# Kernel optimization log

Hardware: AMD Instinct MI355X
Metric: run time of the kernel (lower is better)

## Reference

```python
import jax, jax.numpy as jnp
import numpy as np

H = 16  # num_heads


def setup_inputs() -> dict:
    key = jax.random.key(0)
    ks = jax.random.split(key, 8)
    B, S, d, L = 1, 2048, 1024, 8
    hd = d // H
    s = 0.02
    return {
        "x": jax.random.normal(ks[0], (B, S, d), jnp.float32),
        "past_values": jax.random.normal(ks[1], (L, B, H, S, hd), jnp.float32),
        "Wqkv": jax.random.normal(ks[2], (3 * d, d), jnp.float32) * s,
        "bqkv": jax.random.normal(ks[3], (3 * d,), jnp.float32) * s,
        "Wcol": jax.random.normal(ks[4], (d, d), jnp.float32) * s,
        "bcol": jax.random.normal(ks[5], (d,), jnp.float32) * s,
        "Wout": jax.random.normal(ks[6], (d, d), jnp.float32) * s,
        "bout": jax.random.normal(ks[7], (d,), jnp.float32) * s,
    }


def reference(x, past_values, Wqkv, bqkv, Wcol, bcol, Wout, bout):
    B, S, d = x.shape
    L = past_values.shape[0]
    hd = d // H
    scale = 1.0 / np.sqrt(hd).astype(np.float32)

    qkv = x @ Wqkv.T + bqkv                       # [B,S,3d]
    q, k, v = jnp.split(qkv, 3, axis=-1)

    def heads(t):                                  # [B,S,d] -> [B,H,S,hd]
        return t.reshape(B, S, H, hd).transpose(0, 2, 1, 3)

    q_row, k, v = heads(q), heads(k), heads(v)
    q_col = heads(x @ Wcol.T + bcol)

    # causal token scores [B,H,S,S]
    token_scores = jnp.einsum('bhqd,bhkd->bhqk', q_row, k) * scale
    causal = jnp.triu(jnp.ones((S, S), bool), 1)
    token_scores = jnp.where(causal, -jnp.inf, token_scores)

    # stack past values: torch stack(dim=3) -> [B,H,S,L,hd]; permute -> [B,S,L,H*hd]
    pv = past_values.transpose(1, 3, 0, 2, 4).reshape(B, S, L, d)
    ri = pv.reshape(B, S * L, d)
    mu = ri.mean(-1, keepdims=True)
    var = ri.var(-1, keepdims=True)
    ri = (ri - mu) / jnp.sqrt(var + 1e-5)          # F.layer_norm, no affine

    Wk, bk = Wqkv[d:2 * d], bqkv[d:2 * d]
    Wv, bv = Wqkv[2 * d:], bqkv[2 * d:]
    rk = (ri @ Wk.T + bk).reshape(B, S * L, H, hd).transpose(0, 2, 1, 3).reshape(B, H, S, L, hd)
    rv = (ri @ Wv.T + bv).reshape(B, S * L, H, hd).transpose(0, 2, 1, 3).reshape(B, H, S, L, hd)

    mem_scores = jnp.einsum('bhsd,bhsld->bhsl', q_col, rk) * scale  # [B,H,S,L]

    scores = jnp.concatenate([token_scores, mem_scores], axis=-1)   # [B,H,S,S+L]
    w = jax.nn.softmax(scores, axis=-1)
    tw, mw = w[..., :S], w[..., S:]

    ctx = jnp.einsum('bhqk,bhkd->bhqd', tw, v) + jnp.einsum('bhsl,bhsld->bhsd', mw, rv)
    out = ctx.transpose(0, 2, 1, 3).reshape(B, S, d)
    return out @ Wout.T + bout
```

## Files before the change

kernel.cpp:

```cpp
#include <hip/hip_runtime.h>
#include <math.h>

#define D   1024
#define H   16
#define HD  64
#define SEQ 2048
#define LL  8
#define SCALE 0.125f

typedef __attribute__((ext_vector_type(8))) __bf16 bf16x8;
typedef __attribute__((ext_vector_type(4))) float floatx4;
typedef __attribute__((ext_vector_type(8))) unsigned short ushort8;

__device__ inline unsigned short f32_to_bf16(float f) {
    unsigned int u = __builtin_bit_cast(unsigned int, f);
    u += 0x7FFF + ((u >> 16) & 1);
    return (unsigned short)(u >> 16);
}
__device__ inline float bf2f(unsigned short u) {
    unsigned int x = (unsigned int)u << 16;
    return __builtin_bit_cast(float, x);
}
__device__ inline void load_lds16(const void* g, void* l) {
    __builtin_amdgcn_global_load_lds(
        (__attribute__((address_space(1))) void*)g,
        (__attribute__((address_space(3))) void*)l, 16, 0, 0);
}

__device__ inline void xcd_swizzle(int& bx, int& by) {
    const int gx   = gridDim.x;
    const int lin  = blockIdx.y * gx + blockIdx.x;
    const int nblk = gx * gridDim.y;
    const int virt = (lin & 7) * (nblk >> 3) + (lin >> 3);
    bx = virt % gx;
    by = virt / gx;
}

#define NQ_X    524288
#define NQ_WQKV 786432
#define NQ_WC   262144
#define NQ_WO   262144
#define LN_BLK  16384
#define CVT_BLK 7168
#define PREP_GRID (LN_BLK + CVT_BLK + 4)

__global__ __launch_bounds__(256) void prep_kernel(
    const float* __restrict__ pv, const float* __restrict__ x,
    const float* __restrict__ Wqkv, const float* __restrict__ Wcol,
    const float* __restrict__ Wout, const float* __restrict__ bqkv,
    const float* __restrict__ bcol,
    unsigned short* __restrict__ ri, unsigned short* __restrict__ xb,
    unsigned short* __restrict__ W4b, unsigned short* __restrict__ Woutb,
    float* __restrict__ b4)
{
    const int b = blockIdx.x;
    const int t = threadIdx.x;
    if (b < LN_BLK) {
        const int r = b;
        const int s = r >> 3, l = r & 7;
        const int h = t >> 4, e = (t & 15) * 4;
        const size_t src = (size_t)l * (H * SEQ * HD) + (size_t)h * (SEQ * HD)
                         + (size_t)s * HD + e;
        float4 v = *(const float4*)(pv + src);
        float sum = v.x + v.y + v.z + v.w;
        float sq  = v.x * v.x + v.y * v.y + v.z * v.z + v.w * v.w;
#pragma unroll
        for (int off = 32; off; off >>= 1) {
            sum += __shfl_xor(sum, off);
            sq  += __shfl_xor(sq, off);
        }
        __shared__ float red[8];
        if ((t & 63) == 0) { red[(t >> 6) * 2] = sum; red[(t >> 6) * 2 + 1] = sq; }
        __syncthreads();
        sum = red[0] + red[2] + red[4] + red[6];
        sq  = red[1] + red[3] + red[5] + red[7];
        const float mean = sum * (1.f / 1024.f);
        const float var  = sq * (1.f / 1024.f) - mean * mean;
        const float rstd = rsqrtf(var + 1e-5f);
        ushort4 o;
        o.x = f32_to_bf16((v.x - mean) * rstd);
        o.y = f32_to_bf16((v.y - mean) * rstd);
        o.z = f32_to_bf16((v.z - mean) * rstd);
        o.w = f32_to_bf16((v.w - mean) * rstd);
        *(ushort4*)(ri + (size_t)r * D + t * 4) = o;
    } else if (b < LN_BLK + CVT_BLK) {
        const int i = (b - LN_BLK) * 256 + t;
        const float* src; unsigned short* dst; int off;
        if (i < NQ_X)                        { src = x;    dst = xb;    off = i; }
        else if (i < NQ_X + NQ_WQKV)         { src = Wqkv; dst = W4b;   off = i - NQ_X; }
        else if (i < NQ_X + NQ_WQKV + NQ_WC) { src = Wcol; dst = W4b;   off = i - NQ_X;
                                               src = Wcol; off = i - NQ_X - NQ_WQKV;
                                               dst = W4b + (size_t)NQ_WQKV * 4 / 1;
                                               {
                                                   float4 v = ((const float4*)Wcol)[i - NQ_X - NQ_WQKV];
                                                   ushort4 o;
                                                   o.x = f32_to_bf16(v.x); o.y = f32_to_bf16(v.y);
                                                   o.z = f32_to_bf16(v.z); o.w = f32_to_bf16(v.w);
                                                   ((ushort4*)(W4b))[NQ_WQKV + (i - NQ_X - NQ_WQKV)] = o;
                                               }
                                               return; }
        else                                 { src = Wout; dst = Woutb; off = i - NQ_X - NQ_WQKV - NQ_WC; }
        float4 v = ((const float4*)src)[off];
        ushort4 o;
        o.x = f32_to_bf16(v.x); o.y = f32_to_bf16(v.y);
        o.z = f32_to_bf16(v.z); o.w = f32_to_bf16(v.w);
        ((ushort4*)dst)[off] = o;
    } else {
        const int q = (b - LN_BLK - CVT_BLK) * 256 + t;
        float4 v = (q < 768) ? ((const float4*)bqkv)[q] : ((const float4*)bcol)[q - 768];
        ((float4*)b4)[q] = v;
    }
}

template <typename CT>
__global__ __launch_bounds__(256) void gemm_bf16_kernel(
    const unsigned short* __restrict__ A, const unsigned short* __restrict__ W,
    const float* __restrict__ bias, CT* __restrict__ C, int K, int N)
{
    __shared__ unsigned short As[128 * 32];
    __shared__ unsigned short Ws[128 * 32];
    const int t    = threadIdx.x;
    const int wave = t >> 6, lane = t & 63;
    const int wm   = wave >> 1, wn = wave & 1;
    int bx, by;
    xcd_swizzle(bx, by);
    const int m0 = by * 128, n0 = bx * 128;

    floatx4 acc[4][4];
#pragma unroll
    for (int i = 0; i < 4; i++)
#pragma unroll
        for (int j = 0; j < 4; j++) acc[i][j] = (floatx4)0.f;

    const int lrow = lane >> 2;
    const int lcol = (lane & 3) * 8;
    const unsigned short* Ag = A + (size_t)(m0 + wave * 32 + lrow) * K + lcol;
    const unsigned short* Wg = W + (size_t)(n0 + wave * 32 + lrow) * K + lcol;
    unsigned short* Asw = &As[wave * 32 * 32];
    unsigned short* Wsw = &Ws[wave * 32 * 32];
    const size_t rowskip = (size_t)16 * K;

    const int arow  = lane & 15;
    const int aquad = (lane >> 4) * 8;

    for (int k0 = 0; k0 < K; k0 += 32) {
        load_lds16(Ag + k0,           Asw);
        load_lds16(Ag + k0 + rowskip, Asw + 16 * 32);
        load_lds16(Wg + k0,           Wsw);
        load_lds16(Wg + k0 + rowskip, Wsw + 16 * 32);
        __syncthreads();

        bf16x8 af[4], wf[4];
#pragma unroll
        for (int mi = 0; mi < 4; mi++)
            af[mi] = *(const bf16x8*)&As[(wm * 64 + mi * 16 + arow) * 32 + aquad];
#pragma unroll
        for (int ni = 0; ni < 4; ni++)
            wf[ni] = *(const bf16x8*)&Ws[(wn * 64 + ni * 16 + arow) * 32 + aquad];
#pragma unroll
        for (int mi = 0; mi < 4; mi++)
#pragma unroll
            for (int ni = 0; ni < 4; ni++)
                acc[mi][ni] = __builtin_amdgcn_mfma_f32_16x16x32_bf16(
                    af[mi], wf[ni], acc[mi][ni], 0, 0, 0);
        __syncthreads();
    }

    const int crow = (lane >> 4) * 4, ccol = lane & 15;
#pragma unroll
    for (int mi = 0; mi < 4; mi++) {
#pragma unroll
        for (int ni = 0; ni < 4; ni++) {
            const int gm = m0 + wm * 64 + mi * 16 + crow;
            const int gn = n0 + wn * 64 + ni * 16 + ccol;
            const float bb = bias[gn];
#pragma unroll
            for (int r = 0; r < 4; r++) {
                float v = acc[mi][ni][r] + bb;
                if constexpr (sizeof(CT) == 2)
                    C[(size_t)(gm + r) * N + gn] = (CT)f32_to_bf16(v);
                else
                    C[(size_t)(gm + r) * N + gn] = v;
            }
        }
    }
}

union AttnShared {
    struct { unsigned short Qs[64 * 72]; unsigned short Ks[64 * 72]; } qk;
    float Osp[64 * 68];
};

__global__ __launch_bounds__(256) void attn_split_kernel(
    const unsigned short* __restrict__ qkv4, const unsigned short* __restrict__ rkv,
    float* __restrict__ Opart, float2* __restrict__ mlpart)
{
    const int t    = threadIdx.x;
    const int w    = t >> 6, lane = t & 63;
    const int lrow = lane & 15;
    const int lk   = (lane >> 4) * 8;
    const int rrow = (lane >> 4) * 4;
    const int lin  = blockIdx.x;
    const int hs   = lin & 31, g = lin >> 5;
    const int h    = hs >> 1, s = hs & 1;
    const int a    = g & 7, bq = g >> 3;
    const int qt   = (bq == 0) ? a : (bq == 1) ? 15 - a : (bq == 2) ? 16 + a : 31 - a;
    const int q0   = qt * 64;
    const int n    = qt + 1, nh = (n + 1) >> 1;
    const int lo   = s ? nh : 0, hi = s ? n : nh;
    const int part = (h * 32 + qt) * 2 + s;

    __shared__ AttnShared U;
    __shared__ unsigned short Vt[64 * 72];
    __shared__ unsigned short Pb[64 * 72];
    __shared__ float row_m[64], row_l[64];
    __shared__ float mem_mm[64], mem_alpha[64], mem_suml[64], mem_p[64 * 8];

#pragma unroll
    for (int p = 0; p < 2; p++) {
        int idx = p * 256 + t;
        int row = idx >> 3, col = (idx & 7) * 8;
        *(bf16x8*)&U.qk.Qs[row * 72 + col] =
            *(const bf16x8*)(qkv4 + (size_t)(q0 + row) * 4096 + h * HD + col);
    }

    float m_i[4], l_i[4];
    floatx4 Oacc[4];
#pragma unroll
    for (int r = 0; r < 4; r++) { m_i[r] = -1e30f; l_i[r] = 0.f; }
#pragma unroll
    for (int et = 0; et < 4; et++) Oacc[et] = (floatx4)0.f;

    for (int jt = lo; jt < hi; jt++) {
        const int j0 = jt * 64;
#pragma unroll
        for (int p = 0; p < 2; p++) {
            int idx = p * 256 + t;
            int row = idx >> 3, col = (idx & 7) * 8;
            *(bf16x8*)&U.qk.Ks[row * 72 + col] =
                *(const bf16x8*)(qkv4 + (size_t)(j0 + row) * 4096 + D + h * HD + col);
        }
        {
            const int pr = t & 31, eg = t >> 5;
            const unsigned short* v0 =
                qkv4 + (size_t)(j0 + 2 * pr) * 4096 + 2 * D + h * HD + eg * 8;
            ushort8 va = *(const ushort8*)v0;
            ushort8 vb = *(const ushort8*)(v0 + 4096);
#pragma unroll
            for (int j = 0; j < 8; j++) {
                unsigned int pk = (unsigned int)va[j] | ((unsigned int)vb[j] << 16);
                *(unsigned int*)&Vt[(eg * 8 + j) * 72 + 2 * pr] = pk;
            }
        }
        __syncthreads();

        floatx4 S[4];
#pragma unroll
        for (int nt = 0; nt < 4; nt++) S[nt] = (floatx4)0.f;
#pragma unroll
        for (int kst = 0; kst < 2; kst++) {
            bf16x8 aq = *(const bf16x8*)&U.qk.Qs[(w * 16 + lrow) * 72 + kst * 32 + lk];
#pragma unroll
            for (int nt = 0; nt < 4; nt++) {
                bf16x8 bk = *(const bf16x8*)&U.qk.Ks[(nt * 16 + lrow) * 72 + kst * 32 + lk];
                S[nt] = __builtin_amdgcn_mfma_f32_16x16x32_bf16(aq, bk, S[nt], 0, 0, 0);
            }
        }

#pragma unroll
        for (int r = 0; r < 4; r++) {
            const int qg = q0 + w * 16 + rrow + r;
            float sc[4];
            float mx = -1e30f;
#pragma unroll
            for (int nt = 0; nt < 4; nt++) {
                sc[nt] = S[nt][r] * SCALE;
                if (j0 + nt * 16 + lrow > qg) sc[nt] = -1e30f;
                mx = fmaxf(mx, sc[nt]);
            }
#pragma unroll
            for (int off = 1; off < 16; off <<= 1)
                mx = fmaxf(mx, __shfl_xor(mx, off));
            if (mx <= -1e29f) {
#pragma unroll
                for (int nt = 0; nt < 4; nt++)
                    Pb[(w * 16 + rrow + r) * 72 + nt * 16 + lrow] = 0;
                continue;
            }
            const float newm  = fmaxf(m_i[r], mx);
            const float alpha = __expf(m_i[r] - newm);
            m_i[r] = newm;
            float ps = 0.f;
#pragma unroll
            for (int nt = 0; nt < 4; nt++) {
                float pe = __expf(sc[nt] - newm);
                ps += pe;
                Pb[(w * 16 + rrow + r) * 72 + nt * 16 + lrow] = f32_to_bf16(pe);
            }
#pragma unroll
            for (int off = 1; off < 16; off <<= 1)
                ps += __shfl_xor(ps, off);
            l_i[r] = l_i[r] * alpha + ps;
#pragma unroll
            for (int et = 0; et < 4; et++) Oacc[et][r] *= alpha;
        }
        __syncthreads();

#pragma unroll
        for (int kst = 0; kst < 2; kst++) {
            bf16x8 ap = *(const bf16x8*)&Pb[(w * 16 + lrow) * 72 + kst * 32 + lk];
#pragma unroll
            for (int et = 0; et < 4; et++) {
                bf16x8 bv = *(const bf16x8*)&Vt[(et * 16 + lrow) * 72 + kst * 32 + lk];
                Oacc[et] = __builtin_amdgcn_mfma_f32_16x16x32_bf16(ap, bv, Oacc[et], 0, 0, 0);
            }
        }
        __syncthreads();
    }

    if (s == 1) {
#pragma unroll
        for (int r = 0; r < 4; r++) {
            const int ql = w * 16 + rrow + r;
            if (lrow == 0) mlpart[(size_t)part * 64 + ql] = make_float2(m_i[r], l_i[r]);
#pragma unroll
            for (int et = 0; et < 4; et++)
                Opart[((size_t)part * 64 + ql) * 64 + et * 16 + lrow] = Oacc[et][r];
        }
        return;
    }

#pragma unroll
    for (int r = 0; r < 4; r++) {
        const int ql = w * 16 + rrow + r;
        if (lrow == 0) { row_m[ql] = m_i[r]; row_l[ql] = l_i[r]; }
#pragma unroll
        for (int et = 0; et < 4; et++)
            U.Osp[ql * 68 + et * 16 + lrow] = Oacc[et][r];
    }
    __syncthreads();

    {
        const int qi = t >> 2, quad = t & 3;
        const int qg = q0 + qi;
        float qv[16];
        const unsigned short* qcp = qkv4 + (size_t)qg * 4096 + 3 * D + h * HD + quad * 16;
        ushort8 qa = *(const ushort8*)qcp;
        ushort8 qb = *(const ushort8*)(qcp + 8);
#pragma unroll
        for (int j = 0; j < 8; j++) {
            qv[j]     = bf2f(qa[j]) * SCALE;
            qv[8 + j] = bf2f(qb[j]) * SCALE;
        }
        float ms[8];
#pragma unroll
        for (int l = 0; l < 8; l++) {
            const unsigned short* rr = rkv + (size_t)(qg * LL + l) * 2048 + h * HD + quad * 16;
            ushort8 ra = *(const ushort8*)rr;
            ushort8 rb = *(const ushort8*)(rr + 8);
            float pacc = 0.f;
#pragma unroll
            for (int j = 0; j < 8; j++)
                pacc += qv[j] * bf2f(ra[j]) + qv[8 + j] * bf2f(rb[j]);
            pacc += __shfl_xor(pacc, 1);
            pacc += __shfl_xor(pacc, 2);
            ms[l] = pacc;
        }
        const float mo = row_m[qi];
        float mm = mo;
#pragma unroll
        for (int l = 0; l < 8; l++) mm = fmaxf(mm, ms[l]);
        const float alpha = __expf(mo - mm);
        float suml = 0.f;
        float pl[8];
#pragma unroll
        for (int l = 0; l < 8; l++) { pl[l] = __expf(ms[l] - mm); suml += pl[l]; }
        if (quad == 0) {
            mem_mm[qi]    = mm;
            mem_alpha[qi] = alpha;
            mem_suml[qi]  = suml;
#pragma unroll
            for (int l = 0; l < 8; l++) mem_p[qi * 8 + l] = pl[l];
        }
    }
    __syncthreads();

    {
        const int tx = t & 15, ty = t >> 4;
#pragma unroll
        for (int i = 0; i < 4; i++) {
            const int qi = ty * 4 + i, qg = q0 + qi;
            const float alpha = mem_alpha[qi];
            const float lf = row_l[qi] * alpha + mem_suml[qi];
            float4 o = *(const float4*)&U.Osp[qi * 68 + tx * 4];
            o.x *= alpha; o.y *= alpha; o.z *= alpha; o.w *= alpha;
#pragma unroll
            for (int l = 0; l < 8; l++) {
                const float p = mem_p[qi * 8 + l];
                ushort4 vb = *(const ushort4*)(rkv + (size_t)(qg * LL + l) * 2048
                                               + D + h * HD + tx * 4);
                o.x = fmaf(p, bf2f(vb.x), o.x);
                o.y = fmaf(p, bf2f(vb.y), o.y);
                o.z = fmaf(p, bf2f(vb.z), o.z);
                o.w = fmaf(p, bf2f(vb.w), o.w);
            }
            *(float4*)&Opart[((size_t)part * 64 + qi) * 64 + tx * 4] = o;
            if (tx == 0) mlpart[(size_t)part * 64 + qi] = make_float2(mem_mm[qi], lf);
        }
    }
}

__global__ __launch_bounds__(256) void attn_merge_kernel(
    const float* __restrict__ Opart, const float2* __restrict__ mlpart,
    unsigned short* __restrict__ ctx)
{
    const int blk = blockIdx.x;
    const int h = blk >> 5, qt = blk & 31;
    const int q0 = qt * 64;
    const int t = threadIdx.x, tx = t & 15, ty = t >> 4;
    const size_t p0 = (size_t)blk * 2, p1 = p0 + 1;
#pragma unroll
    for (int i = 0; i < 4; i++) {
        const int qi = ty * 4 + i, qg = q0 + qi;
        float2 ml0 = mlpart[p0 * 64 + qi];
        float2 ml1 = mlpart[p1 * 64 + qi];
        const float M  = fmaxf(ml0.x, ml1.x);
        const float f0 = __expf(ml0.x - M), f1 = __expf(ml1.x - M);
        const float rl = 1.f / (ml0.y * f0 + ml1.y * f1);
        float4 o0 = *(const float4*)&Opart[(p0 * 64 + qi) * 64 + tx * 4];
        float4 o1 = *(const float4*)&Opart[(p1 * 64 + qi) * 64 + tx * 4];
        ushort4 ob;
        ob.x = f32_to_bf16((o0.x * f0 + o1.x * f1) * rl);
        ob.y = f32_to_bf16((o0.y * f0 + o1.y * f1) * rl);
        ob.z = f32_to_bf16((o0.z * f0 + o1.z * f1) * rl);
        ob.w = f32_to_bf16((o0.w * f0 + o1.w * f1) * rl);
        *(ushort4*)(ctx + (size_t)qg * D + h * HD + tx * 4) = ob;
    }
}

extern "C" void kernel_launch(void* const* d_in, const int* in_sizes, int n_in,
                              void* d_out, int out_size, void* d_ws, size_t ws_size,
                              hipStream_t stream)
{
    const float* x    = (const float*)d_in[0];
    const float* pv   = (const float*)d_in[1];
    const float* Wqkv = (const float*)d_in[2];
    const float* bqkv = (const float*)d_in[3];
    const float* Wcol = (const float*)d_in[4];
    const float* bcol = (const float*)d_in[5];
    const float* Wout = (const float*)d_in[6];
    const float* bout = (const float*)d_in[7];
    float* out = (float*)d_out;

    char* p = (char*)d_ws;
    unsigned short* x_bf    = (unsigned short*)p; p += (size_t)2048 * 1024 * 2;
    unsigned short* W4_bf   = (unsigned short*)p; p += (size_t)4096 * 1024 * 2;
    unsigned short* Wout_bf = (unsigned short*)p; p += (size_t)1024 * 1024 * 2;
    float*          b4      = (float*)p;          p += (size_t)4096 * 4;
    unsigned short* ri_bf   = (unsigned short*)p; p += (size_t)16384 * 1024 * 2;
    unsigned short* qkv4_bf = (unsigned short*)p; p += (size_t)2048 * 4096 * 2;
    unsigned short* rkv_bf  = (unsigned short*)p; p += (size_t)16384 * 2048 * 2;
    unsigned short* ctx_bf  = (unsigned short*)p; p += (size_t)2048 * 1024 * 2;
    float*          Opart   = (float*)p;          p += (size_t)1024 * 64 * 64 * 4;
    float2*         mlpart  = (float2*)p;         p += (size_t)1024 * 64 * 8;

    prep_kernel<<<PREP_GRID, 256, 0, stream>>>(pv, x, Wqkv, Wcol, Wout, bqkv, bcol,
                                               ri_bf, x_bf, W4_bf, Wout_bf, b4);
    gemm_bf16_kernel<unsigned short><<<dim3(32, 16), 256, 0, stream>>>(
        x_bf, W4_bf, b4, qkv4_bf, 1024, 4096);
    gemm_bf16_kernel<unsigned short><<<dim3(16, 128), 256, 0, stream>>>(
        ri_bf, W4_bf + (size_t)1024 * 1024, bqkv + 1024, rkv_bf, 1024, 2048);
    attn_split_kernel<<<1024, 256, 0, stream>>>(qkv4_bf, rkv_bf, Opart, mlpart);
    attn_merge_kernel<<<512, 256, 0, stream>>>(Opart, mlpart, ctx_bf);
    gemm_bf16_kernel<float><<<dim3(8, 16), 256, 0, stream>>>(
        ctx_bf, Wout_bf, bout, out, 1024, 1024);
}
```

Baseline: 363.4 us.

## Fold memory K/V projections into attention via reassociation, drop rkv GEMM

Removes the large GEMM that projected all 16384 layer-normed past rows to K and V. A new mem_attn kernel instead folds Wk into the query (q·Wk_h, precomputed with a transposed Wk) and computes memory scores directly against the normalized rows. It then applies the softmax weights to those rows before multiplying by Wv, with bias terms handled analytically. The memory branch gets its own max/sum and is merged with the two token-attention partials in the merge kernel. This trades a 16384x2048x1024 GEMM and its large intermediate for smaller per-block MFMA work and an extra transpose in prep. The risk is large register arrays (z0/z1 of 64 floats each) and repeated reads of ri.

New measurement: 370.0 us. Within noise of the previous version (+1.8%).

```diff
diff --git a/kernel.cpp b/kernel.cpp
--- a/kernel.cpp
+++ b/kernel.cpp
@@ -7,6 +7,7 @@
 #define SEQ 2048
 #define LL  8
 #define SCALE 0.125f
+#define TZS 1048
 
 typedef __attribute__((ext_vector_type(8))) __bf16 bf16x8;
 typedef __attribute__((ext_vector_type(4))) float floatx4;
@@ -26,7 +27,6 @@
         (__attribute__((address_space(1))) void*)g,
         (__attribute__((address_space(3))) void*)l, 16, 0, 0);
 }
-
 __device__ inline void xcd_swizzle(int& bx, int& by) {
     const int gx   = gridDim.x;
     const int lin  = blockIdx.y * gx + blockIdx.x;
@@ -39,10 +39,10 @@
 #define NQ_X    524288
 #define NQ_WQKV 786432
 #define NQ_WC   262144
-#define NQ_WO   262144
 #define LN_BLK  16384
 #define CVT_BLK 7168
-#define PREP_GRID (LN_BLK + CVT_BLK + 4)
+#define TR_BLK  256
+#define PREP_GRID (LN_BLK + CVT_BLK + 4 + TR_BLK)
 
 __global__ __launch_bounds__(256) void prep_kernel(
     const float* __restrict__ pv, const float* __restrict__ x,
@@ -51,8 +51,9 @@
     const float* __restrict__ bcol,
     unsigned short* __restrict__ ri, unsigned short* __restrict__ xb,
     unsigned short* __restrict__ W4b, unsigned short* __restrict__ Woutb,
-    float* __restrict__ b4)
+    float* __restrict__ b4, unsigned short* __restrict__ WkT)
 {
+    __shared__ float ft[64][65];
     const int b = blockIdx.x;
     const int t = threadIdx.x;
     if (b < LN_BLK) {
@@ -86,29 +87,46 @@
     } else if (b < LN_BLK + CVT_BLK) {
         const int i = (b - LN_BLK) * 256 + t;
         const float* src; unsigned short* dst; int off;
-        if (i < NQ_X)                        { src = x;    dst = xb;    off = i; }
-        else if (i < NQ_X + NQ_WQKV)         { src = Wqkv; dst = W4b;   off = i - NQ_X; }
-        else if (i < NQ_X + NQ_WQKV + NQ_WC) { src = Wcol; dst = W4b;   off = i - NQ_X;
-                                               src = Wcol; off = i - NQ_X - NQ_WQKV;
-                                               dst = W4b + (size_t)NQ_WQKV * 4 / 1;
-                                               {
-                                                   float4 v = ((const float4*)Wcol)[i - NQ_X - NQ_WQKV];
-                                                   ushort4 o;
-                                                   o.x = f32_to_bf16(v.x); o.y = f32_to_bf16(v.y);
-                                                   o.z = f32_to_bf16(v.z); o.w = f32_to_bf16(v.w);
-                                                   ((ushort4*)(W4b))[NQ_WQKV + (i - NQ_X - NQ_WQKV)] = o;
-                                               }
-                                               return; }
-        else                                 { src = Wout; dst = Woutb; off = i - NQ_X - NQ_WQKV - NQ_WC; }
+        if (i < NQ_X) {
+            src = x; dst = xb; off = i;
+        } else if (i < NQ_X + NQ_WQKV) {
+            src = Wqkv; dst = W4b; off = i - NQ_X;
+        } else if (i < NQ_X + NQ_WQKV + NQ_WC) {
+            src = Wcol; dst = W4b + (size_t)NQ_WQKV * 4; off = i - NQ_X - NQ_WQKV;
+        } else {
+            src = Wout; dst = Woutb; off = i - NQ_X - NQ_WQKV - NQ_WC;
+        }
         float4 v = ((const float4*)src)[off];
         ushort4 o;
         o.x = f32_to_bf16(v.x); o.y = f32_to_bf16(v.y);
         o.z = f32_to_bf16(v.z); o.w = f32_to_bf16(v.w);
         ((ushort4*)dst)[off] = o;
-    } else {
+    } else if (b < LN_BLK + CVT_BLK + 4) {
         const int q = (b - LN_BLK - CVT_BLK) * 256 + t;
         float4 v = (q < 768) ? ((const float4*)bqkv)[q] : ((const float4*)bcol)[q - 768];
         ((float4*)b4)[q] = v;
+    } else {
+        const int tt = b - LN_BLK - CVT_BLK - 4;
+        const int kt = tt >> 4, et = tt & 15;
+        const int r = t >> 2, c16 = (t & 3) * 16;
+        const float* srow = Wqkv + (size_t)(1024 + et * 64 + r) * 1024 + kt * 64 + c16;
+#pragma unroll
+        for (int j = 0; j < 4; j++) {
+            float4 v = *(const float4*)(srow + j * 4);
+            ft[r][c16 + j * 4 + 0] = v.x; ft[r][c16 + j * 4 + 1] = v.y;
+            ft[r][c16 + j * 4 + 2] = v.z; ft[r][c16 + j * 4 + 3] = v.w;
+        }
+        __syncthreads();
+        const int rk = t >> 2, ec = (t & 3) * 16;
+        unsigned short* orow = WkT + (size_t)(kt * 64 + rk) * 1024 + et * 64 + ec;
+#pragma unroll
+        for (int half = 0; half < 2; half++) {
+            ushort8 o;
+#pragma unroll
+            for (int j = 0; j < 8; j++)
+                o[j] = f32_to_bf16(ft[ec + half * 8 + j][rk]);
+            *(ushort8*)(orow + half * 8) = o;
+        }
     }
 }
 
@@ -186,13 +204,186 @@
     }
 }
 
-union AttnShared {
-    struct { unsigned short Qs[64 * 72]; unsigned short Ks[64 * 72]; } qk;
-    float Osp[64 * 68];
-};
+__global__ __launch_bounds__(256, 2) void mem_attn_kernel(
+    const unsigned short* __restrict__ qkv4, const unsigned short* __restrict__ ri,
+    const unsigned short* __restrict__ WkT, const unsigned short* __restrict__ Wv,
+    const float* __restrict__ bk, const float* __restrict__ bv,
+    float* __restrict__ Omem, float2* __restrict__ mlmem)
+{
+    const int t = threadIdx.x;
+    const int w = t >> 6, lane = t & 63;
+    const int lrow = lane & 15, quad = lane >> 4, lk = quad * 8;
+    const int b  = blockIdx.x;
+    const int sg = (b & 7) + 8 * ((b >> 3) & 15);
+    const int hg = b >> 7;
+    const int s0 = sg * 16;
+    const int r0 = s0 * 8;
+
+    __shared__ unsigned short tz[2][16][TZS];
+    __shared__ float s_sc[2][16][8];
+    __shared__ float s_c[2][16];
+    __shared__ float s_p[2][16][8];
+    __shared__ float s_l2[2][16];
+
+    {
+        const int hh = t >> 7, s = (t >> 3) & 15, g = t & 7;
+        const int h = hg * 2 + hh;
+        const unsigned short* qc = qkv4 + (size_t)(s0 + s) * 4096 + 3072 + h * 64 + g * 8;
+        ushort8 qv = *(const ushort8*)qc;
+        float acc = 0.f;
+#pragma unroll
+        for (int j = 0; j < 8; j++)
+            acc += bf2f(qv[j]) * bk[h * 64 + g * 8 + j];
+        acc += __shfl_xor(acc, 1);
+        acc += __shfl_xor(acc, 2);
+        acc += __shfl_xor(acc, 4);
+        if (g == 0) s_c[hh][s] = acc;
+    }
+
+    bf16x8 aq[2][2];
+#pragma unroll
+    for (int hh = 0; hh < 2; hh++)
+#pragma unroll
+        for (int kst = 0; kst < 2; kst++)
+            aq[hh][kst] = *(const bf16x8*)(qkv4 + (size_t)(s0 + lrow) * 4096 + 3072
+                                           + (hg * 2 + hh) * 64 + kst * 32 + lk);
+#pragma unroll
+    for (int hh = 0; hh < 2; hh++) {
+        const int h = hg * 2 + hh;
+#pragma unroll
+        for (int nt = 0; nt < 16; nt++) {
+            const int n = w * 256 + nt * 16;
+            floatx4 acc = (floatx4)0.f;
+#pragma unroll
+            for (int kst = 0; kst < 2; kst++) {
+                bf16x8 bw = *(const bf16x8*)(WkT + (size_t)(n + lrow) * 1024
+                                             + h * 64 + kst * 32 + lk);
+                acc = __builtin_amdgcn_mfma_f32_16x16x32_bf16(aq[hh][kst], bw, acc, 0, 0, 0);
+            }
+#pragma unroll
+            for (int r = 0; r < 4; r++)
+                tz[hh][quad * 4 + r][n + lrow] = f32_to_bf16(acc[r]);
+        }
+    }
+    __syncthreads();
+
+    {
+        floatx4 sacc[2][2];
+#pragma unroll
+        for (int ntl = 0; ntl < 2; ntl++)
+#pragma unroll
+            for (int hh = 0; hh < 2; hh++) sacc[ntl][hh] = (floatx4)0.f;
+        for (int kst = 0; kst < 32; kst++) {
+            bf16x8 at0 = *(const bf16x8*)&tz[0][lrow][kst * 32 + lk];
+            bf16x8 at1 = *(const bf16x8*)&tz[1][lrow][kst * 32 + lk];
+#pragma unroll
+            for (int ntl = 0; ntl < 2; ntl++) {
+                bf16x8 br = *(const bf16x8*)(ri + (size_t)(r0 + w * 32 + ntl * 16 + lrow) * 1024
+                                             + kst * 32 + lk);
+                sacc[ntl][0] = __builtin_amdgcn_mfma_f32_16x16x32_bf16(at0, br, sacc[ntl][0], 0, 0, 0);
+                sacc[ntl][1] = __builtin_amdgcn_mfma_f32_16x16x32_bf16(at1, br, sacc[ntl][1], 0, 0, 0);
+            }
+        }
+        if (quad == w) {
+            const int l = lrow & 7, hi = (lrow >> 3) & 1;
+#pragma unroll
+            for (int ntl = 0; ntl < 2; ntl++) {
+                const int s = 4 * w + 2 * ntl + hi;
+#pragma unroll
+                for (int hh = 0; hh < 2; hh++) {
+                    float val = hi ? sacc[ntl][hh][2 * ntl + 1] : sacc[ntl][hh][2 * ntl];
+                    s_sc[hh][s][l] = val;
+                }
+            }
+        }
+    }
+    __syncthreads();
+
+    if (t < 32) {
+        const int hh = t >> 4, s = t & 15;
+        const int h = hg * 2 + hh;
+        const float c = s_c[hh][s];
+        float sc[8], m2 = -1e30f;
+#pragma unroll
+        for (int l = 0; l < 8; l++) {
+            sc[l] = (s_sc[hh][s][l] + c) * SCALE;
+            m2 = fmaxf(m2, sc[l]);
+        }
+        float l2 = 0.f;
+#pragma unroll
+        for (int l = 0; l < 8; l++) {
+            float p = __expf(sc[l] - m2);
+            s_p[hh][s][l] = p;
+            l2 += p;
+        }
+        s_l2[hh][s] = l2;
+        mlmem[(size_t)h * 2048 + s0 + s] = make_float2(m2, l2);
+    }
+    __syncthreads();
+
+    {
+        const int s = t & 15, kc = (t >> 4) * 64;
+        float z0[64], z1[64];
+#pragma unroll
+        for (int j = 0; j < 64; j++) { z0[j] = 0.f; z1[j] = 0.f; }
+        for (int l = 0; l < 8; l++) {
+            const float p0 = s_p[0][s][l], p1 = s_p[1][s][l];
+            const unsigned short* base = ri + (size_t)(r0 + s * 8 + l) * 1024 + kc;
+#pragma unroll
+            for (int c8 = 0; c8 < 8; c8++) {
+                ushort8 v = *(const ushort8*)(base + c8 * 8);
+#pragma unroll
+                for (int j = 0; j < 8; j++) {
+                    float f = bf2f(v[j]);
+                    z0[c8 * 8 + j] = fmaf(p0, f, z0[c8 * 8 + j]);
+                    z1[c8 * 8 + j] = fmaf(p1, f, z1[c8 * 8 + j]);
+                }
+            }
+        }
+        __syncthreads();
+#pragma unroll
+        for (int c8 = 0; c8 < 8; c8++) {
+            ushort8 o0, o1;
+#pragma unroll
+            for (int j = 0; j < 8; j++) {
+                o0[j] = f32_to_bf16(z0[c8 * 8 + j]);
+                o1[j] = f32_to_bf16(z1[c8 * 8 + j]);
+            }
+            *(ushort8*)&tz[0][s][kc + c8 * 8] = o0;
+            *(ushort8*)&tz[1][s][kc + c8 * 8] = o1;
+        }
+    }
+    __syncthreads();
+
+    {
+        floatx4 oacc[2] = {(floatx4)0.f, (floatx4)0.f};
+        for (int kst = 0; kst < 32; kst++) {
+            bf16x8 az0 = *(const bf16x8*)&tz[0][lrow][kst * 32 + lk];
+            bf16x8 az1 = *(const bf16x8*)&tz[1][lrow][kst * 32 + lk];
+            bf16x8 bw0 = *(const bf16x8*)(Wv + (size_t)((hg * 2 + 0) * 64 + w * 16 + lrow) * 1024
+                                          + kst * 32 + lk);
+            bf16x8 bw1 = *(const bf16x8*)(Wv + (size_t)((hg * 2 + 1) * 64 + w * 16 + lrow) * 1024
+                                          + kst * 32 + lk);
+            oacc[0] = __builtin_amdgcn_mfma_f32_16x16x32_bf16(az0, bw0, oacc[0], 0, 0, 0);
+            oacc[1] = __builtin_amdgcn_mfma_f32_16x16x32_bf16(az1, bw1, oacc[1], 0, 0, 0);
+        }
+        const int e = w * 16 + lrow;
+#pragma unroll
+        for (int hh = 0; hh < 2; hh++) {
+            const int h = hg * 2 + hh;
+            const float bve = bv[h * 64 + e];
+#pragma unroll
+            for (int r = 0; r < 4; r++) {
+                const int s = quad * 4 + r;
+                Omem[((size_t)h * 2048 + s0 + s) * 64 + e] =
+                    oacc[hh][r] + s_l2[hh][s] * bve;
+            }
+        }
+    }
+}
 
 __global__ __launch_bounds__(256) void attn_split_kernel(
-    const unsigned short* __restrict__ qkv4, const unsigned short* __restrict__ rkv,
+    const unsigned short* __restrict__ qkv4,
     float* __restrict__ Opart, float2* __restrict__ mlpart)
 {
     const int t    = threadIdx.x;
@@ -210,17 +401,16 @@
     const int lo   = s ? nh : 0, hi = s ? n : nh;
     const int part = (h * 32 + qt) * 2 + s;
 
-    __shared__ AttnShared U;
+    __shared__ unsigned short Qs[64 * 72];
+    __shared__ unsigned short Ks[64 * 72];
     __shared__ unsigned short Vt[64 * 72];
     __shared__ unsigned short Pb[64 * 72];
-    __shared__ float row_m[64], row_l[64];
-    __shared__ float mem_mm[64], mem_alpha[64], mem_suml[64], mem_p[64 * 8];
 
 #pragma unroll
     for (int p = 0; p < 2; p++) {
         int idx = p * 256 + t;
         int row = idx >> 3, col = (idx & 7) * 8;
-        *(bf16x8*)&U.qk.Qs[row * 72 + col] =
+        *(bf16x8*)&Qs[row * 72 + col] =
             *(const bf16x8*)(qkv4 + (size_t)(q0 + row) * 4096 + h * HD + col);
     }
 
@@ -237,7 +427,7 @@
         for (int p = 0; p < 2; p++) {
             int idx = p * 256 + t;
             int row = idx >> 3, col = (idx & 7) * 8;
-            *(bf16x8*)&U.qk.Ks[row * 72 + col] =
+            *(bf16x8*)&Ks[row * 72 + col] =
                 *(const bf16x8*)(qkv4 + (size_t)(j0 + row) * 4096 + D + h * HD + col);
         }
         {
@@ -259,11 +449,11 @@
         for (int nt = 0; nt < 4; nt++) S[nt] = (floatx4)0.f;
 #pragma unroll
         for (int kst = 0; kst < 2; kst++) {
-            bf16x8 aq = *(const bf16x8*)&U.qk.Qs[(w * 16 + lrow) * 72 + kst * 32 + lk];
+            bf16x8 aqf = *(const bf16x8*)&Qs[(w * 16 + lrow) * 72 + kst * 32 + lk];
 #pragma unroll
             for (int nt = 0; nt < 4; nt++) {
-                bf16x8 bk = *(const bf16x8*)&U.qk.Ks[(nt * 16 + lrow) * 72 + kst * 32 + lk];
-                S[nt] = __builtin_amdgcn_mfma_f32_16x16x32_bf16(aq, bk, S[nt], 0, 0, 0);
+                bf16x8 bk = *(const bf16x8*)&Ks[(nt * 16 + lrow) * 72 + kst * 32 + lk];
+                S[nt] = __builtin_amdgcn_mfma_f32_16x16x32_bf16(aqf, bk, S[nt], 0, 0, 0);
             }
         }
 
@@ -318,100 +508,19 @@
         __syncthreads();
     }
 
-    if (s == 1) {
-#pragma unroll
-        for (int r = 0; r < 4; r++) {
-            const int ql = w * 16 + rrow + r;
-            if (lrow == 0) mlpart[(size_t)part * 64 + ql] = make_float2(m_i[r], l_i[r]);
-#pragma unroll
-            for (int et = 0; et < 4; et++)
-                Opart[((size_t)part * 64 + ql) * 64 + et * 16 + lrow] = Oacc[et][r];
-        }
-        return;
-    }
-
 #pragma unroll
     for (int r = 0; r < 4; r++) {
         const int ql = w * 16 + rrow + r;
-        if (lrow == 0) { row_m[ql] = m_i[r]; row_l[ql] = l_i[r]; }
+        if (lrow == 0) mlpart[(size_t)part * 64 + ql] = make_float2(m_i[r], l_i[r]);
 #pragma unroll
         for (int et = 0; et < 4; et++)
-            U.Osp[ql * 68 + et * 16 + lrow] = Oacc[et][r];
-    }
-    __syncthreads();
-
-    {
-        const int qi = t >> 2, quad = t & 3;
-        const int qg = q0 + qi;
-        float qv[16];
-        const unsigned short* qcp = qkv4 + (size_t)qg * 4096 + 3 * D + h * HD + quad * 16;
-        ushort8 qa = *(const ushort8*)qcp;
-        ushort8 qb = *(const ushort8*)(qcp + 8);
-#pragma unroll
-        for (int j = 0; j < 8; j++) {
-            qv[j]     = bf2f(qa[j]) * SCALE;
-            qv[8 + j] = bf2f(qb[j]) * SCALE;
-        }
-        float ms[8];
-#pragma unroll
-        for (int l = 0; l < 8; l++) {
-            const unsigned short* rr = rkv + (size_t)(qg * LL + l) * 2048 + h * HD + quad * 16;
-            ushort8 ra = *(const ushort8*)rr;
-            ushort8 rb = *(const ushort8*)(rr + 8);
-            float pacc = 0.f;
-#pragma unroll
-            for (int j = 0; j < 8; j++)
-                pacc += qv[j] * bf2f(ra[j]) + qv[8 + j] * bf2f(rb[j]);
-            pacc += __shfl_xor(pacc, 1);
-            pacc += __shfl_xor(pacc, 2);
-            ms[l] = pacc;
-        }
-        const float mo = row_m[qi];
-        float mm = mo;
-#pragma unroll
-        for (int l = 0; l < 8; l++) mm = fmaxf(mm, ms[l]);
-        const float alpha = __expf(mo - mm);
-        float suml = 0.f;
-        float pl[8];
-#pragma unroll
-        for (int l = 0; l < 8; l++) { pl[l] = __expf(ms[l] - mm); suml += pl[l]; }
-        if (quad == 0) {
-            mem_mm[qi]    = mm;
-            mem_alpha[qi] = alpha;
-            mem_suml[qi]  = suml;
-#pragma unroll
-            for (int l = 0; l < 8; l++) mem_p[qi * 8 + l] = pl[l];
-        }
-    }
-    __syncthreads();
-
-    {
-        const int tx = t & 15, ty = t >> 4;
-#pragma unroll
-        for (int i = 0; i < 4; i++) {
-            const int qi = ty * 4 + i, qg = q0 + qi;
-            const float alpha = mem_alpha[qi];
-            const float lf = row_l[qi] * alpha + mem_suml[qi];
-            float4 o = *(const float4*)&U.Osp[qi * 68 + tx * 4];
-            o.x *= alpha; o.y *= alpha; o.z *= alpha; o.w *= alpha;
-#pragma unroll
-            for (int l = 0; l < 8; l++) {
-                const float p = mem_p[qi * 8 + l];
-                ushort4 vb = *(const ushort4*)(rkv + (size_t)(qg * LL + l) * 2048
-                                               + D + h * HD + tx * 4);
-                o.x = fmaf(p, bf2f(vb.x), o.x);
-                o.y = fmaf(p, bf2f(vb.y), o.y);
-                o.z = fmaf(p, bf2f(vb.z), o.z);
-                o.w = fmaf(p, bf2f(vb.w), o.w);
-            }
-            *(float4*)&Opart[((size_t)part * 64 + qi) * 64 + tx * 4] = o;
-            if (tx == 0) mlpart[(size_t)part * 64 + qi] = make_float2(mem_mm[qi], lf);
-        }
+            Opart[((size_t)part * 64 + ql) * 64 + et * 16 + lrow] = Oacc[et][r];
     }
 }
 
 __global__ __launch_bounds__(256) void attn_merge_kernel(
     const float* __restrict__ Opart, const float2* __restrict__ mlpart,
+    const float* __restrict__ Omem, const float2* __restrict__ mlmem,
     unsigned short* __restrict__ ctx)
 {
     const int blk = blockIdx.x;
@@ -424,16 +533,18 @@
         const int qi = ty * 4 + i, qg = q0 + qi;
         float2 ml0 = mlpart[p0 * 64 + qi];
         float2 ml1 = mlpart[p1 * 64 + qi];
-        const float M  = fmaxf(ml0.x, ml1.x);
-        const float f0 = __expf(ml0.x - M), f1 = __expf(ml1.x - M);
-        const float rl = 1.f / (ml0.y * f0 + ml1.y * f1);
+        float2 mlm = mlmem[(size_t)h * 2048 + qg];
+        const float M  = fmaxf(fmaxf(ml0.x, ml1.x), mlm.x);
+        const float f0 = __expf(ml0.x - M), f1 = __expf(ml1.x - M), fm = __expf(mlm.x - M);
+        const float rl = 1.f / (ml0.y * f0 + ml1.y * f1 + mlm.y * fm);
         float4 o0 = *(const float4*)&Opart[(p0 * 64 + qi) * 64 + tx * 4];
         float4 o1 = *(const float4*)&Opart[(p1 * 64 + qi) * 64 + tx * 4];
+        float4 om = *(const float4*)&Omem[((size_t)h * 2048 + qg) * 64 + tx * 4];
         ushort4 ob;
-        ob.x = f32_to_bf16((o0.x * f0 + o1.x * f1) * rl);
-        ob.y = f32_to_bf16((o0.y * f0 + o1.y * f1) * rl);
-        ob.z = f32_to_bf16((o0.z * f0 + o1.z * f1) * rl);
-        ob.w = f32_to_bf16((o0.w * f0 + o1.w * f1) * rl);
+        ob.x = f32_to_bf16((o0.x * f0 + o1.x * f1 + om.x * fm) * rl);
+        ob.y = f32_to_bf16((o0.y * f0 + o1.y * f1 + om.y * fm) * rl);
+        ob.z = f32_to_bf16((o0.z * f0 + o1.z * f1 + om.z * fm) * rl);
+        ob.w = f32_to_bf16((o0.w * f0 + o1.w * f1 + om.w * fm) * rl);
         *(ushort4*)(ctx + (size_t)qg * D + h * HD + tx * 4) = ob;
     }
 }
@@ -457,21 +568,24 @@
     unsigned short* W4_bf   = (unsigned short*)p; p += (size_t)4096 * 1024 * 2;
     unsigned short* Wout_bf = (unsigned short*)p; p += (size_t)1024 * 1024 * 2;
     float*          b4      = (float*)p;          p += (size_t)4096 * 4;
+    unsigned short* WkT_bf  = (unsigned short*)p; p += (size_t)1024 * 1024 * 2;
     unsigned short* ri_bf   = (unsigned short*)p; p += (size_t)16384 * 1024 * 2;
     unsigned short* qkv4_bf = (unsigned short*)p; p += (size_t)2048 * 4096 * 2;
-    unsigned short* rkv_bf  = (unsigned short*)p; p += (size_t)16384 * 2048 * 2;
     unsigned short* ctx_bf  = (unsigned short*)p; p += (size_t)2048 * 1024 * 2;
     float*          Opart   = (float*)p;          p += (size_t)1024 * 64 * 64 * 4;
     float2*         mlpart  = (float2*)p;         p += (size_t)1024 * 64 * 8;
+    float*          Omem    = (float*)p;          p += (size_t)16 * 2048 * 64 * 4;
+    float2*         mlmem   = (float2*)p;         p += (size_t)16 * 2048 * 8;
 
     prep_kernel<<<PREP_GRID, 256, 0, stream>>>(pv, x, Wqkv, Wcol, Wout, bqkv, bcol,
-                                               ri_bf, x_bf, W4_bf, Wout_bf, b4);
+                                               ri_bf, x_bf, W4_bf, Wout_bf, b4, WkT_bf);
     gemm_bf16_kernel<unsigned short><<<dim3(32, 16), 256, 0, stream>>>(
         x_bf, W4_bf, b4, qkv4_bf, 1024, 4096);
-    gemm_bf16_kernel<unsigned short><<<dim3(16, 128), 256, 0, stream>>>(
-        ri_bf, W4_bf + (size_t)1024 * 1024, bqkv + 1024, rkv_bf, 1024, 2048);
-    attn_split_kernel<<<1024, 256, 0, stream>>>(qkv4_bf, rkv_bf, Opart, mlpart);
-    attn_merge_kernel<<<512, 256, 0, stream>>>(Opart, mlpart, ctx_bf);
+    attn_split_kernel<<<1024, 256, 0, stream>>>(qkv4_bf, Opart, mlpart);
+    mem_attn_kernel<<<1024, 256, 0, stream>>>(
+        qkv4_bf, ri_bf, WkT_bf, W4_bf + (size_t)2048 * 1024,
+        bqkv + 1024, bqkv + 2048, Omem, mlmem);
+    attn_merge_kernel<<<512, 256, 0, stream>>>(Opart, mlpart, Omem, mlmem, ctx_bf);
     gemm_bf16_kernel<float><<<dim3(8, 16), 256, 0, stream>>>(
         ctx_bf, Wout_bf, bout, out, 1024, 1024);
 }
```
